# Kernel tuning notes

Hardware: AMD Instinct MI355X
Metric: run time of the kernel (lower is better)

The kernel has to match this reference:

```python
import jax, jax.numpy as jnp
import numpy as np

B, N, D, K = 4, 2048, 128, 32
EPS = 1e-5  # nn.LayerNorm default eps


def _lin(k, fan_in, fan_out):
    kw, kb = jax.random.split(k)
    s = 1.0 / np.sqrt(fan_in)
    w = jax.random.uniform(kw, (fan_in, fan_out), jnp.float32, -s, s)
    b = jax.random.uniform(kb, (fan_out,), jnp.float32, -s, s)
    return w, b


def setup_inputs() -> dict:
    key = jax.random.key(0)
    ks = jax.random.split(key, 3)
    inp = {}
    inp["features"] = jax.random.normal(ks[0], (B, N, D), jnp.float32)
    inp["coords"] = jax.random.uniform(ks[1], (B, N, 3), jnp.float32) * 64.0
    names = [("ql", D, D), ("kl", D, D), ("vl", D, D), ("pl1", 3, D), ("pl2", D, D),
             ("we1", D, D), ("we2", D, D), ("pe1", 3, D), ("pe2", D, D),
             ("sg1", D, D), ("sg2", D, D)]
    k2 = jax.random.split(ks[2], len(names))
    for (nm, fi, fo), kk in zip(names, k2):
        w, b = _lin(kk, fi, fo)
        inp[nm + "_w"] = w
        inp[nm + "_b"] = b
    inp["lnA_g"] = jnp.ones((D,), jnp.float32)
    inp["lnA_b"] = jnp.zeros((D,), jnp.float32)
    inp["lnF_g"] = jnp.ones((D,), jnp.float32)
    inp["lnF_b"] = jnp.zeros((D,), jnp.float32)
    return inp


def _sparsemax_k(z):
    # sparsemax over axis=1 (the K neighbor axis) of [N, K, D]
    zs = -jnp.sort(-z, axis=1)                      # descending sort
    zc = jnp.cumsum(zs, axis=1)
    r = jnp.arange(1, K + 1, dtype=z.dtype)[None, :, None]
    support = (r * zs) > (zc - 1.0)
    kz = jnp.sum(support, axis=1, keepdims=True).astype(jnp.int32)  # >= 1
    tau = (jnp.take_along_axis(zc, kz - 1, axis=1) - 1.0) / kz.astype(z.dtype)
    return jnp.maximum(z - tau, 0.0)


def _sg_prop(x, src, tgt, n):
    # SGConv (K=1) propagation: D^{-1/2}(A+I)D^{-1/2} x with self-loops added
    ar = jnp.arange(n)
    s = jnp.concatenate([src, ar])
    t = jnp.concatenate([tgt, ar])
    deg = jax.ops.segment_sum(jnp.ones(s.shape, x.dtype), t, num_segments=n)
    dinv = jax.lax.rsqrt(deg)
    norm = dinv[s] * dinv[t]
    return jax.ops.segment_sum(x[s] * norm[:, None], t, num_segments=n)


def reference(features, coords,
              ql_w, ql_b, kl_w, kl_b, vl_w, vl_b,
              pl1_w, pl1_b, pl2_w, pl2_b,
              we1_w, we1_b, we2_w, we2_b,
              lnA_g, lnA_b,
              pe1_w, pe1_b, pe2_w, pe2_b,
              sg1_w, sg1_b, sg2_w, sg2_b,
              lnF_g, lnF_b):
    def ln(x, g, b):
        m = jnp.mean(x, axis=-1, keepdims=True)
        v = jnp.var(x, axis=-1, keepdims=True)
        return (x - m) * jax.lax.rsqrt(v + EPS) * g + b

    def one(feat, coord):
        # ---- RNSA: KNN self-attention with positional embedding ----
        d2 = jnp.sum((coord[:, None, :] - coord[None, :, :]) ** 2, axis=-1)  # [N,N]
        _, idx = jax.lax.top_k(-d2, K)                   # [N,K], self included first
        diff = coord[idx] - coord[:, None, :]            # [N,K,3]
        fc = jnp.maximum(diff @ pl1_w + pl1_b, 0.0) @ pl2_w + pl2_b  # [N,K,D]
        pe = fc + feat[idx]
        Q = jnp.maximum(feat @ ql_w + ql_b, 0.0)         # [N,D]
        Kf = jnp.maximum(pe @ kl_w + kl_b, 0.0)          # [N,K,D]
        V = pe @ vl_w + vl_b
        rel = (Kf - Q[:, None, :]) * fc
        w = jnp.maximum(rel @ we1_w + we1_b, 0.0) @ we2_w + we2_b
        w = _sparsemax_k(w)                              # attn_drop is identity (eval)
        x_att = feat + jnp.einsum('nkd,nkd->nd', V, w)   # residual add
        cf = jnp.maximum(coord @ pe1_w + pe1_b, 0.0) @ pe2_w + pe2_b
        x_in = ln(x_att, lnA_g, lnA_b)
        x_pe = x_in + cf
        d2m = d2 + jnp.where(jnp.eye(N, dtype=bool), jnp.inf, 0.0)  # knn_graph: loop=False
        _, idx2 = jax.lax.top_k(-d2m, K)                 # [N,K] neighbors (sources)
        src = idx2.reshape(-1)
        tgt = jnp.repeat(jnp.arange(N), K)
        h = _sg_prop(x_pe, src, tgt, N) @ sg1_w + sg1_b
        h = jnp.maximum(h, 0.0)
        h = _sg_prop(h, src, tgt, N) @ sg2_w + sg2_b     # dropout is identity (eval)
        return ln(h + x_in, lnF_g, lnF_b)

    return jax.vmap(one)(features, coords)
```

## Files before the change

kernel.cpp:

```cpp
#include <hip/hip_runtime.h>
#include <hip/hip_bf16.h>


namespace {
constexpr int BB = 4;
constexpr int NN = 2048;
constexpr int DD = 128;
constexpr int KK = 32;
constexpr float LNEPS = 1e-5f;
constexpr int SH = 136;

constexpr int W_QL = 0, W_KL = 16384, W_VL = 32768, W_PL2 = 49152, W_WE1 = 65536,
              W_WE2 = 81920, W_PE2 = 98304, W_SG1 = 114688, W_SG2 = 131072,
              W_PL1 = 147456, W_PE1 = 147840,
              B_QL = 148224, B_KL = 148352, B_VL = 148480, B_PL1 = 148608, B_PL2 = 148736,
              B_WE1 = 148864, B_WE2 = 148992, B_PE1 = 149120, B_PE2 = 149248,
              B_SG1 = 149376, B_SG2 = 149504,
              LNA_G = 149632, LNA_B = 149760, LNF_G = 149888, LNF_B = 150016;

constexpr long OFF_FEAT  = 0;
constexpr long OFF_Q     = 1l << 20;
constexpr long OFF_XIN   = 3l << 20;
constexpr long OFF_XPE   = 4l << 20;
constexpr long OFF_H1    = 5l << 20;
constexpr long OFF_COORD = 6l << 20;
constexpr long OFF_W     = (6l << 20) + 32768;
constexpr long OFF_IDX   = (6l << 20) + 262144;
}

typedef _Float16 f16;
typedef __attribute__((ext_vector_type(8))) _Float16 half8;
typedef __attribute__((ext_vector_type(4))) float f32x4;

struct WPtrs { const void* p[26]; };

__device__ __forceinline__ f32x4 mfma16h(half8 a, half8 b, f32x4 c) {
  return __builtin_amdgcn_mfma_f32_16x16x32_f16(a, b, c, 0, 0, 0);
}
__device__ __forceinline__ bool bf_inputs(const unsigned* __restrict__ dt) {
  return (dt[0] & 0xFFFFu) != 0u;
}

__global__ __launch_bounds__(256) void k_prep(WPtrs wp,
    const void* __restrict__ feat, const void* __restrict__ coord,
    const unsigned* __restrict__ dt,
    float* __restrict__ featf, float* __restrict__ coordf, float* __restrict__ Wf,
    f16* __restrict__ pkH, f16* __restrict__ pkL) {
  const bool isbf = bf_inputs(dt);
  const int tid = threadIdx.x;
  if (blockIdx.x < 2048) {
    const int nf = BB * NN * DD, nc = BB * NN * 3;
    for (int i = blockIdx.x * 256 + tid; i < nf + nc; i += 2048 * 256) {
      if (i < nf) {
        featf[i] = isbf ? __bfloat162float(((const __hip_bfloat16*)feat)[i])
                        : ((const float*)feat)[i];
      } else {
        const int j = i - nf;
        coordf[j] = isbf ? __bfloat162float(((const __hip_bfloat16*)coord)[j])
                         : ((const float*)coord)[j];
      }
    }
  } else if (blockIdx.x < 2048 + 26) {
    const int sizes[26] = {16384,16384,16384,16384,16384,16384,16384,16384,16384,
                           384,384,
                           128,128,128,128,128,128,128,128,128,128,128,
                           128,128,128,128};
    const int offs[26] = {W_QL,W_KL,W_VL,W_PL2,W_WE1,W_WE2,W_PE2,W_SG1,W_SG2,
                          W_PL1,W_PE1,
                          B_QL,B_KL,B_VL,B_PL1,B_PL2,B_WE1,B_WE2,B_PE1,B_PE2,B_SG1,B_SG2,
                          LNA_G,LNA_B,LNF_G,LNF_B};
    const int t = blockIdx.x - 2048;
    float* dst = Wf + offs[t];
    const int n = sizes[t];
    if (isbf) {
      const __hip_bfloat16* src = (const __hip_bfloat16*)wp.p[t];
      for (int i = tid; i < n; i += 256) dst[i] = __bfloat162float(src[i]);
    } else {
      const float* src = (const float*)wp.p[t];
      for (int i = tid; i < n; i += 256) dst[i] = src[i];
    }
  } else {
    const int wmap[9] = {3, 1, 2, 4, 5, 6, 7, 8, 0};
    const int m = blockIdx.x - 2048 - 26;
    const void* src = wp.p[wmap[m]];
    f16* H = pkH + m * 16384;
    f16* L = pkL + m * 16384;
    for (int f = tid; f < 16384; f += 256) {
      const int j = f & 7, lane = (f >> 3) & 63, ks = (f >> 9) & 3, nt = f >> 11;
      const int k = ks * 32 + ((lane >> 4) << 3) + j, n = nt * 16 + (lane & 15);
      const float v = isbf ? __bfloat162float(((const __hip_bfloat16*)src)[k * 128 + n])
                           : ((const float*)src)[k * 128 + n];
      const f16 h = (f16)v;
      H[f] = h;
      L[f] = (f16)(v - (float)h);
    }
  }
}

__device__ __forceinline__ void mm_core(const f16* sA,
                                        const f16* __restrict__ wH,
                                        const f16* __restrict__ wL,
                                        bool useLoW, int lane, int wv, f32x4 acc[2][2]) {
  const int colq = lane & 15, quad = lane >> 4;
  #pragma unroll
  for (int mt = 0; mt < 2; ++mt) {
    const int arow = mt * 16 + colq;
    f32x4 a0 = {0.f, 0.f, 0.f, 0.f}, a1 = {0.f, 0.f, 0.f, 0.f};
    #pragma unroll
    for (int ks = 0; ks < 4; ++ks) {
      const half8 a = *(const half8*)(sA + arow * SH + ks * 32 + quad * 8);
      const int nt0 = 2 * wv, nt1 = 2 * wv + 1;
      const half8 b0 = *(const half8*)(wH + ((nt0 * 4 + ks) * 64 + lane) * 8);
      const half8 b1 = *(const half8*)(wH + ((nt1 * 4 + ks) * 64 + lane) * 8);
      a0 = mfma16h(a, b0, a0);
      a1 = mfma16h(a, b1, a1);
      if (useLoW) {
        const half8 bl0 = *(const half8*)(wL + ((nt0 * 4 + ks) * 64 + lane) * 8);
        const half8 bl1 = *(const half8*)(wL + ((nt1 * 4 + ks) * 64 + lane) * 8);
        a0 = mfma16h(a, bl0, a0);
        a1 = mfma16h(a, bl1, a1);
      }
    }
    acc[mt][0] = a0;
    acc[mt][1] = a1;
  }
}

__device__ __forceinline__ void h_store2(f16* A, int row0, int col, float v0, float v1) {
  A[row0 * SH + col] = (f16)v0;
  A[(row0 + 1) * SH + col] = (f16)v1;
}

__device__ __forceinline__ void h_store_row16(f16* A, int row, int c0, const float* v) {
  half8 o0, o1;
  #pragma unroll
  for (int e = 0; e < 8; ++e) { o0[e] = (f16)v[e]; o1[e] = (f16)v[8 + e]; }
  *(half8*)(A + row * SH + c0) = o0;
  *(half8*)(A + row * SH + c0 + 8) = o1;
}

__global__ __launch_bounds__(256) void k_knn_q(const float* __restrict__ coordf,
                                               const float* __restrict__ featf,
                                               const float* __restrict__ Wf,
                                               const f16* __restrict__ pkH,
                                               const f16* __restrict__ pkL,
                                               const unsigned* __restrict__ dt,
                                               int* __restrict__ idx1, int* __restrict__ idx2,
                                               float* __restrict__ Qm) {
  __shared__ __align__(16) unsigned char smem[NN * 3 * 4 + 4 * 33 * 4];
  const int tid = threadIdx.x;
  if (blockIdx.x < 2048) {
    float* cs = (float*)smem;
    int (*tops)[33] = (int(*)[33])(smem + NN * 3 * 4);
    const int wv = tid >> 6, lane = tid & 63;
    const int blk = blockIdx.x;
    const int b = blk >> 9;
    const int i = ((blk & 511) << 2) + wv;
    const float* cb = coordf + (long)b * NN * 3;
    for (int t = tid; t < NN * 3 / 4; t += 256) ((float4*)cs)[t] = ((const float4*)cb)[t];
    __syncthreads();
    const float qx = cs[i*3+0], qy = cs[i*3+1], qz = cs[i*3+2];
    float v[32];
    unsigned removed = 0u;
    float m1v = 1e30f, m2v = 1e30f; int m1j = 0x7fffffff, m2j = 0x7fffffff;
    #pragma unroll
    for (int m = 0; m < 32; m++) {
      const int j = m * 64 + lane;
      const float dx = cs[j*3+0] - qx, dy = cs[j*3+1] - qy, dz = cs[j*3+2] - qz;
      const float d2 = __fadd_rn(__fadd_rn(__fmul_rn(dx,dx), __fmul_rn(dy,dy)), __fmul_rn(dz,dz));
      v[m] = d2;
      if (d2 < m1v)      { m2v = m1v; m2j = m1j; m1v = d2; m1j = j; }
      else if (d2 < m2v) { m2v = d2; m2j = j; }
    }
    bool dirty = false;
    for (int s = 0; s < 33; s++) {
      float mv = m1v; int mj = m1j;
      #pragma unroll
      for (int off = 1; off < 64; off <<= 1) {
        const float ov = __shfl_xor(mv, off, 64);
        const int   oj = __shfl_xor(mj, off, 64);
        if (ov < mv || (ov == mv && oj < mj)) { mv = ov; mj = oj; }
      }
      if (lane == 0) tops[wv][s] = mj;
      if ((mj & 63) == lane) {
        removed |= 1u << (mj >> 6);
        if (!dirty) { m1v = m2v; m1j = m2j; dirty = true; }
        else {
          m1v = 1e30f; m1j = 0x7fffffff; m2v = 1e30f; m2j = 0x7fffffff;
          #pragma unroll
          for (int m = 0; m < 32; m++) {
            if (!((removed >> m) & 1u)) {
              const float d2 = v[m]; const int j = m * 64 + lane;
              if (d2 < m1v)      { m2v = m1v; m2j = m1j; m1v = d2; m1j = j; }
              else if (d2 < m2v) { m2v = d2; m2j = j; }
            }
          }
          dirty = false;
        }
      }
    }
    const unsigned long long sm = __ballot(lane < 33 && tops[wv][lane] == i);
    const int p = sm ? (__ffsll((long long)sm) - 1) : 32;
    if (lane < KK) {
      const long g = (long)b * NN + i;
      idx1[g * KK + lane] = tops[wv][lane];
      idx2[g * KK + lane] = tops[wv][lane + (lane >= p ? 1 : 0)];
    }
  } else {
    f16* AH = (f16*)smem;
    const int lane = tid & 63, wv = tid >> 6;
    const int colq = lane & 15, quad = lane >> 4;
    const bool useLoW = !bf_inputs(dt);
    const int row8 = tid >> 3, c0 = (tid & 7) * 16;
    const long gg0 = (long)(blockIdx.x - 2048) * 32;
    float s[16];
    const float* sp = featf + (gg0 + row8) * DD + c0;
    #pragma unroll
    for (int e = 0; e < 16; e += 4) {
      const float4 vv = *(const float4*)(sp + e);
      s[e] = vv.x; s[e+1] = vv.y; s[e+2] = vv.z; s[e+3] = vv.w;
    }
    h_store_row16(AH, row8, c0, s);
    __syncthreads();
    f32x4 acc[2][2];
    mm_core(AH, pkH + 8*16384, pkL + 8*16384, useLoW, lane, wv, acc);
    #pragma unroll
    for (int ntl = 0; ntl < 2; ++ntl) {
      const int col = (2*wv + ntl)*16 + colq;
      const float bv = Wf[B_QL + col];
      #pragma unroll
      for (int mt = 0; mt < 2; ++mt) {
        const int rowb = mt*16 + quad*4;
        #pragma unroll
        for (int r = 0; r < 4; ++r)
          Qm[(gg0 + rowb + r) * DD + col] = fmaxf(acc[mt][ntl][r] + bv, 0.f);
      }
    }
  }
}

__global__ __launch_bounds__(256, 4) void k_attn(const float* __restrict__ featf,
                                              const float* __restrict__ coordf,
                                              const float* __restrict__ Qm,
                                              const int* __restrict__ idx1,
                                              const float* __restrict__ Wf,
                                              const f16* __restrict__ pkH,
                                              const f16* __restrict__ pkL,
                                              const unsigned* __restrict__ dt,
                                              float* __restrict__ x_in) {
  __shared__ __align__(16) f16 AH[KK*SH], CH[KK*SH];
  __shared__ int nb[KK];
  const int tid = threadIdx.x;
  const int lane = tid & 63, wv = tid >> 6;
  const int colq = lane & 15, quad = lane >> 4;
  const int g = blockIdx.x; const int i = g & (NN - 1); const int b = g >> 11;
  const long bN = (long)b * NN;
  const bool useLoW = !bf_inputs(dt);
  if (tid < KK) nb[tid] = idx1[(long)g * KK + tid];
  const int row8 = tid >> 3, c0 = (tid & 7) * 16;

  {
    const int j = idx1[(long)g * KK + row8];
    const float* cb = coordf + (long)b * NN * 3;
    const float dx = cb[j*3+0] - cb[i*3+0], dy = cb[j*3+1] - cb[i*3+1], dz = cb[j*3+2] - cb[i*3+2];
    float t1v[16];
    #pragma unroll
    for (int c4 = 0; c4 < 4; ++c4) {
      const int cc = c0 + c4*4;
      const float4 w0 = *(const float4*)(Wf + W_PL1 + cc);
      const float4 w1 = *(const float4*)(Wf + W_PL1 + 128 + cc);
      const float4 w2 = *(const float4*)(Wf + W_PL1 + 256 + cc);
      const float4 bp = *(const float4*)(Wf + B_PL1 + cc);
      t1v[c4*4+0] = fmaxf(fmaf(dz,w2.x,fmaf(dy,w1.x,fmaf(dx,w0.x,bp.x))), 0.f);
      t1v[c4*4+1] = fmaxf(fmaf(dz,w2.y,fmaf(dy,w1.y,fmaf(dx,w0.y,bp.y))), 0.f);
      t1v[c4*4+2] = fmaxf(fmaf(dz,w2.z,fmaf(dy,w1.z,fmaf(dx,w0.z,bp.z))), 0.f);
      t1v[c4*4+3] = fmaxf(fmaf(dz,w2.w,fmaf(dy,w1.w,fmaf(dx,w0.w,bp.w))), 0.f);
    }
    h_store_row16(AH, row8, c0, t1v);
  }
  __syncthreads();
  f32x4 acc[2][2];
  float fc[2][2][4];
  {
    float pfeat[2][2][4];
    #pragma unroll
    for (int ntl = 0; ntl < 2; ++ntl) {
      const int col = (2*wv + ntl)*16 + colq;
      #pragma unroll
      for (int mt = 0; mt < 2; ++mt) {
        const int rowb = mt*16 + quad*4;
        #pragma unroll
        for (int r = 0; r < 4; ++r)
          pfeat[ntl][mt][r] = featf[(bN + nb[rowb + r]) * DD + col];
      }
    }
    mm_core(AH, pkH + 0*16384, pkL + 0*16384, useLoW, lane, wv, acc);
    #pragma unroll
    for (int ntl = 0; ntl < 2; ++ntl) {
      const int col = (2*wv + ntl)*16 + colq;
      const float bv = Wf[B_PL2 + col];
      #pragma unroll
      for (int mt = 0; mt < 2; ++mt) {
        const int rowb = mt*16 + quad*4;
        float pe[4];
        #pragma unroll
        for (int r = 0; r < 4; ++r) {
          const float f = acc[mt][ntl][r] + bv;
          fc[mt][ntl][r] = f;
          pe[r] = f + pfeat[ntl][mt][r];
        }
        h_store2(CH, rowb + 0, col, pe[0], pe[1]);
        h_store2(CH, rowb + 2, col, pe[2], pe[3]);
      }
    }
  }
  __syncthreads();
  {
    const float qv0 = Qm[(bN + i) * DD + (2*wv + 0)*16 + colq];
    const float qv1 = Qm[(bN + i) * DD + (2*wv + 1)*16 + colq];
    mm_core(CH, pkH + 1*16384, pkL + 1*16384, useLoW, lane, wv, acc);
    #pragma unroll
    for (int ntl = 0; ntl < 2; ++ntl) {
      const int col = (2*wv + ntl)*16 + colq;
      const float bv = Wf[B_KL + col];
      const float qv = ntl ? qv1 : qv0;
      #pragma unroll
      for (int mt = 0; mt < 2; ++mt) {
        const int rowb = mt*16 + quad*4;
        float rel[4];
        #pragma unroll
        for (int r = 0; r < 4; ++r) {
          const float kf = fmaxf(acc[mt][ntl][r] + bv, 0.f);
          rel[r] = (kf - qv) * fc[mt][ntl][r];
        }
        h_store2(AH, rowb + 0, col, rel[0], rel[1]);
        h_store2(AH, rowb + 2, col, rel[2], rel[3]);
      }
    }
  }
  f32x4 Vacc[2][2];
  mm_core(CH, pkH + 2*16384, pkL + 2*16384, useLoW, lane, wv, Vacc);
  __syncthreads();
  {
    mm_core(AH, pkH + 3*16384, pkL + 3*16384, useLoW, lane, wv, acc);
    #pragma unroll
    for (int ntl = 0; ntl < 2; ++ntl) {
      const int col = (2*wv + ntl)*16 + colq;
      const float bv = Wf[B_WE1 + col];
      #pragma unroll
      for (int mt = 0; mt < 2; ++mt) {
        const int rowb = mt*16 + quad*4;
        h_store2(CH, rowb + 0, col,
                 fmaxf(acc[mt][ntl][0] + bv, 0.f), fmaxf(acc[mt][ntl][1] + bv, 0.f));
        h_store2(CH, rowb + 2, col,
                 fmaxf(acc[mt][ntl][2] + bv, 0.f), fmaxf(acc[mt][ntl][3] + bv, 0.f));
      }
    }
  }
  __syncthreads();
  float* XR = (float*)AH;
  const float res0 = featf[(bN + i) * DD + (2*wv + 0)*16 + colq];
  const float res1 = featf[(bN + i) * DD + (2*wv + 1)*16 + colq];
  f32x4 Wacc[2][2];
  mm_core(CH, pkH + 4*16384, pkL + 4*16384, useLoW, lane, wv, Wacc);

  #pragma unroll
  for (int ntl = 0; ntl < 2; ++ntl) {
    const int col = (2*wv + ntl)*16 + colq;
    const float bw = Wf[B_WE2 + col];
    const float bvv = Wf[B_VL + col];
    float z[8], Vv[8];
    #pragma unroll
    for (int mt = 0; mt < 2; ++mt)
      #pragma unroll
      for (int r = 0; r < 4; ++r) {
        z[mt*4+r]  = Wacc[mt][ntl][r] + bw;
        Vv[mt*4+r] = Vacc[mt][ntl][r] + bvv;
      }
    float S = 0.f;
    #pragma unroll
    for (int e = 0; e < 8; ++e) S += z[e];
    S += __shfl_xor(S, 16, 64); S += __shfl_xor(S, 32, 64);
    float tau = (S - 1.0f) * (1.0f / 32.0f);
    int cnt = 32;
    for (int it = 0; it < 40; ++it) {
      float s = 0.f; int c = 0;
      #pragma unroll
      for (int e = 0; e < 8; ++e) { if (z[e] > tau) { s += z[e]; c++; } }
      s += __shfl_xor(s, 16, 64); s += __shfl_xor(s, 32, 64);
      c += __shfl_xor(c, 16, 64); c += __shfl_xor(c, 32, 64);
      const float ntau = (s - 1.0f) / (float)c;
      const int changed = (c != cnt);
      cnt = c; tau = ntau;
      if (!__any(changed)) break;
    }
    float pv = 0.f;
    #pragma unroll
    for (int e = 0; e < 8; ++e) pv = fmaf(fmaxf(z[e] - tau, 0.f), Vv[e], pv);
    pv += __shfl_xor(pv, 16, 64); pv += __shfl_xor(pv, 32, 64);
    if (quad == 0) XR[col] = (ntl ? res1 : res0) + pv;
  }
  __syncthreads();
  {
    const float xa0 = XR[2*lane], xa1 = XR[2*lane + 1];
    float sm = xa0 + xa1;
    float s2 = fmaf(xa0, xa0, xa1 * xa1);
    #pragma unroll
    for (int off = 1; off < 64; off <<= 1) {
      sm += __shfl_xor(sm, off, 64);
      s2 += __shfl_xor(s2, off, 64);
    }
    const float m = sm * (1.f/128.f);
    const float var = s2 * (1.f/128.f) - m * m;
    const float rstd = rsqrtf(var + LNEPS);
    if (tid < DD) {
      const float xin = (XR[tid] - m) * rstd * Wf[LNA_G + tid] + Wf[LNA_B + tid];
      x_in[(bN + i) * DD + tid] = xin;
    }
  }
}

__global__ __launch_bounds__(256) void k_pe(const float* __restrict__ x_in,
                                            const float* __restrict__ coordf,
                                            const float* __restrict__ Wf,
                                            const f16* __restrict__ pkH,
                                            const f16* __restrict__ pkL,
                                            const unsigned* __restrict__ dt,
                                            float* __restrict__ x_pe) {
  __shared__ __align__(16) f16 AH[KK*SH];
  const int tid = threadIdx.x;
  const int lane = tid & 63, wv = tid >> 6;
  const int colq = lane & 15, quad = lane >> 4;
  const bool useLoW = !bf_inputs(dt);
  const int row8 = tid >> 3, c0 = (tid & 7) * 16;
  const long gg0 = (long)blockIdx.x * 32;
  const long gr = gg0 + row8;
  const int b = (int)(gr >> 11), i = (int)(gr & (NN - 1));

  {
    const float* cp = coordf + ((long)b * NN + i) * 3;
    const float cx = cp[0], cy = cp[1], cz = cp[2];
    float tv[16];
    #pragma unroll
    for (int c4 = 0; c4 < 4; ++c4) {
      const int cc = c0 + c4*4;
      const float4 w0 = *(const float4*)(Wf + W_PE1 + cc);
      const float4 w1 = *(const float4*)(Wf + W_PE1 + 128 + cc);
      const float4 w2 = *(const float4*)(Wf + W_PE1 + 256 + cc);
      const float4 bp = *(const float4*)(Wf + B_PE1 + cc);
      tv[c4*4+0] = fmaxf(fmaf(cz,w2.x,fmaf(cy,w1.x,fmaf(cx,w0.x,bp.x))), 0.f);
      tv[c4*4+1] = fmaxf(fmaf(cz,w2.y,fmaf(cy,w1.y,fmaf(cx,w0.y,bp.y))), 0.f);
      tv[c4*4+2] = fmaxf(fmaf(cz,w2.z,fmaf(cy,w1.z,fmaf(cx,w0.z,bp.z))), 0.f);
      tv[c4*4+3] = fmaxf(fmaf(cz,w2.w,fmaf(cy,w1.w,fmaf(cx,w0.w,bp.w))), 0.f);
    }
    h_store_row16(AH, row8, c0, tv);
  }
  __syncthreads();
  f32x4 acc[2][2];
  mm_core(AH, pkH + 5*16384, pkL + 5*16384, useLoW, lane, wv, acc);
  #pragma unroll
  for (int ntl = 0; ntl < 2; ++ntl) {
    const int col = (2*wv + ntl)*16 + colq;
    const float bv = Wf[B_PE2 + col];
    #pragma unroll
    for (int mt = 0; mt < 2; ++mt) {
      const int rowb = mt*16 + quad*4;
      #pragma unroll
      for (int r = 0; r < 4; ++r)
        x_pe[(gg0 + rowb + r) * DD + col] =
            x_in[(gg0 + rowb + r) * DD + col] + acc[mt][ntl][r] + bv;
    }
  }
}

__global__ __launch_bounds__(256) void k_sg1(const float* __restrict__ x_pe,
                                             const int* __restrict__ idx2,
                                             const float* __restrict__ Wf,
                                             const f16* __restrict__ pkH,
                                             const f16* __restrict__ pkL,
                                             const unsigned* __restrict__ dt,
                                             float* __restrict__ h1) {
  __shared__ __align__(16) f16 AH[KK*SH];
  __shared__ int nb2[32][KK];
  const int tid = threadIdx.x;
  const int lane = tid & 63, wv = tid >> 6;
  const int colq = lane & 15, quad = lane >> 4;
  const bool useLoW = !bf_inputs(dt);
  const int row8 = tid >> 3, c0 = (tid & 7) * 16;
  const long gg0 = (long)blockIdx.x * 32;
  const long bN = (gg0 >> 11) << 11;
  for (int t = tid; t < 32 * KK; t += 256)
    nb2[t >> 5][t & 31] = idx2[(gg0 + (t >> 5)) * KK + (t & 31)];
  __syncthreads();
  float s[16];
  {
    const float* sp = x_pe + (gg0 + row8) * DD + c0;
    #pragma unroll
    for (int e = 0; e < 16; e += 4) {
      const float4 v = *(const float4*)(sp + e);
      s[e] = v.x; s[e+1] = v.y; s[e+2] = v.z; s[e+3] = v.w;
    }
  }
  for (int k = 0; k < KK; ++k) {
    const float* np_ = x_pe + (bN + nb2[row8][k]) * DD + c0;
    #pragma unroll
    for (int e = 0; e < 16; e += 4) {
      const float4 v = *(const float4*)(np_ + e);
      s[e] += v.x; s[e+1] += v.y; s[e+2] += v.z; s[e+3] += v.w;
    }
  }
  #pragma unroll
  for (int e = 0; e < 16; ++e) s[e] *= (1.f / 33.f);
  h_store_row16(AH, row8, c0, s);
  __syncthreads();
  f32x4 acc[2][2];
  mm_core(AH, pkH + 6*16384, pkL + 6*16384, useLoW, lane, wv, acc);
  #pragma unroll
  for (int ntl = 0; ntl < 2; ++ntl) {
    const int col = (2*wv + ntl)*16 + colq;
    const float bv = Wf[B_SG1 + col];
    #pragma unroll
    for (int mt = 0; mt < 2; ++mt) {
      const int rowb = mt*16 + quad*4;
      #pragma unroll
      for (int r = 0; r < 4; ++r)
        h1[(gg0 + rowb + r) * DD + col] = fmaxf(acc[mt][ntl][r] + bv, 0.f);
    }
  }
}

__global__ __launch_bounds__(256) void k_sg2(const float* __restrict__ h1,
                                             const int* __restrict__ idx2,
                                             const float* __restrict__ x_in,
                                             const float* __restrict__ Wf,
                                             const f16* __restrict__ pkH,
                                             const f16* __restrict__ pkL,
                                             const unsigned* __restrict__ dt,
                                             void* __restrict__ out) {
  __shared__ __align__(16) f16 AH[KK*SH];
  __shared__ float Yf[KK][132];
  __shared__ int nb2[32][KK];
  const int tid = threadIdx.x;
  const int lane = tid & 63, wv = tid >> 6;
  const int colq = lane & 15, quad = lane >> 4;
  const bool isbf = bf_inputs(dt);
  const bool useLoW = !isbf;
  const int row8 = tid >> 3, c0 = (tid & 7) * 16;
  const long gg0 = (long)blockIdx.x * 32;
  const long bN = (gg0 >> 11) << 11;
  for (int t = tid; t < 32 * KK; t += 256)
    nb2[t >> 5][t & 31] = idx2[(gg0 + (t >> 5)) * KK + (t & 31)];
  __syncthreads();
  float s[16];
  {
    const float* sp = h1 + (gg0 + row8) * DD + c0;
    #pragma unroll
    for (int e = 0; e < 16; e += 4) {
      const float4 v = *(const float4*)(sp + e);
      s[e] = v.x; s[e+1] = v.y; s[e+2] = v.z; s[e+3] = v.w;
    }
  }
  for (int k = 0; k < KK; ++k) {
    const float* np_ = h1 + (bN + nb2[row8][k]) * DD + c0;
    #pragma unroll
    for (int e = 0; e < 16; e += 4) {
      const float4 v = *(const float4*)(np_ + e);
      s[e] += v.x; s[e+1] += v.y; s[e+2] += v.z; s[e+3] += v.w;
    }
  }
  #pragma unroll
  for (int e = 0; e < 16; ++e) s[e] *= (1.f / 33.f);
  h_store_row16(AH, row8, c0, s);
  __syncthreads();
  f32x4 acc[2][2];
  mm_core(AH, pkH + 7*16384, pkL + 7*16384, useLoW, lane, wv, acc);
  #pragma unroll
  for (int ntl = 0; ntl < 2; ++ntl) {
    const int col = (2*wv + ntl)*16 + colq;
    const float bv = Wf[B_SG2 + col];
    #pragma unroll
    for (int mt = 0; mt < 2; ++mt) {
      const int rowb = mt*16 + quad*4;
      #pragma unroll
      for (int r = 0; r < 4; ++r)
        Yf[rowb + r][col] = acc[mt][ntl][r] + bv + x_in[(gg0 + rowb + r) * DD + col];
    }
  }
  __syncthreads();
  float y[16];
  #pragma unroll
  for (int e = 0; e < 16; ++e) y[e] = Yf[row8][c0 + e];
  float sm = 0.f, s2 = 0.f;
  #pragma unroll
  for (int e = 0; e < 16; ++e) { sm += y[e]; s2 = fmaf(y[e], y[e], s2); }
  #pragma unroll
  for (int off = 1; off < 8; off <<= 1) {
    sm += __shfl_xor(sm, off, 64);
    s2 += __shfl_xor(s2, off, 64);
  }
  const float m = sm * (1.f/128.f);
  const float var = s2 * (1.f/128.f) - m * m;
  const float rstd = rsqrtf(var + LNEPS);
  const long gr = gg0 + row8;
  #pragma unroll
  for (int e = 0; e < 16; ++e) {
    const float o = (y[e] - m) * rstd * Wf[LNF_G + c0 + e] + Wf[LNF_B + c0 + e];
    if (isbf) ((__hip_bfloat16*)out)[gr * DD + c0 + e] = __float2bfloat16(o);
    else      ((float*)out)[gr * DD + c0 + e] = o;
  }
}

extern "C" void kernel_launch(void* const* d_in, const int* in_sizes, int n_in,
                              void* d_out, int out_size, void* d_ws, size_t ws_size,
                              hipStream_t stream) {
  float* ws = (float*)d_ws;
  float* featf  = ws + OFF_FEAT;
  float* Qm     = ws + OFF_Q;
  float* x_in   = ws + OFF_XIN;
  float* x_pe   = ws + OFF_XPE;
  float* h1     = ws + OFF_H1;
  float* coordf = ws + OFF_COORD;
  float* Wf     = ws + OFF_W;
  int* idx1 = (int*)(ws + OFF_IDX);
  int* idx2 = idx1 + (long)BB * NN * KK;
  f16* pkH = (f16*)(idx2 + (long)BB * NN * KK);
  f16* pkL = pkH + 9 * 16384;
  const unsigned* dt = (const unsigned*)d_in[24];

  WPtrs wp;
  const int map[26] = {2,4,6,10,12,14,18,20,22, 8,16,
                       3,5,7,9,11,13,15,17,19,21,23,
                       24,25,26,27};
  for (int t = 0; t < 26; t++) wp.p[t] = d_in[map[t]];

  k_prep<<<2048 + 26 + 9, 256, 0, stream>>>(wp, d_in[0], d_in[1], dt,
                                            featf, coordf, Wf, pkH, pkL);
  k_knn_q<<<BB * NN / 4 + BB * NN / 32, 256, 0, stream>>>(coordf, featf, Wf, pkH, pkL, dt,
                                                          idx1, idx2, Qm);
  k_attn<<<BB * NN, 256, 0, stream>>>(featf, coordf, Qm, idx1, Wf, pkH, pkL, dt, x_in);
  k_pe<<<BB * NN / 32, 256, 0, stream>>>(x_in, coordf, Wf, pkH, pkL, dt, x_pe);
  k_sg1<<<BB * NN / 32, 256, 0, stream>>>(x_pe, idx2, Wf, pkH, pkL, dt, h1);
  k_sg2<<<BB * NN / 32, 256, 0, stream>>>(h1, idx2, x_in, Wf, pkH, pkL, dt, (void*)d_out);
}
```

Baseline: 460.2 us.

## Move KNN search into prep kernel, split Q projection into its own kernel

```diff
diff --git a/kernel.cpp b/kernel.cpp
--- a/kernel.cpp
+++ b/kernel.cpp
@@ -45,7 +45,9 @@
     const void* __restrict__ feat, const void* __restrict__ coord,
     const unsigned* __restrict__ dt,
     float* __restrict__ featf, float* __restrict__ coordf, float* __restrict__ Wf,
-    f16* __restrict__ pkH, f16* __restrict__ pkL) {
+    f16* __restrict__ pkH, f16* __restrict__ pkL,
+    int* __restrict__ idx1, int* __restrict__ idx2) {
+  __shared__ __align__(16) unsigned char smem[NN * 3 * 4 + 4 * 33 * 4];
   const bool isbf = bf_inputs(dt);
   const int tid = threadIdx.x;
   if (blockIdx.x < 2048) {
@@ -79,7 +81,7 @@
       const float* src = (const float*)wp.p[t];
       for (int i = tid; i < n; i += 256) dst[i] = src[i];
     }
-  } else {
+  } else if (blockIdx.x < 2048 + 26 + 9) {
     const int wmap[9] = {3, 1, 2, 4, 5, 6, 7, 8, 0};
     const int m = blockIdx.x - 2048 - 26;
     const void* src = wp.p[wmap[m]];
@@ -94,70 +96,27 @@
       H[f] = h;
       L[f] = (f16)(v - (float)h);
     }
-  }
-}
-
-__device__ __forceinline__ void mm_core(const f16* sA,
-                                        const f16* __restrict__ wH,
-                                        const f16* __restrict__ wL,
-                                        bool useLoW, int lane, int wv, f32x4 acc[2][2]) {
-  const int colq = lane & 15, quad = lane >> 4;
-  #pragma unroll
-  for (int mt = 0; mt < 2; ++mt) {
-    const int arow = mt * 16 + colq;
-    f32x4 a0 = {0.f, 0.f, 0.f, 0.f}, a1 = {0.f, 0.f, 0.f, 0.f};
-    #pragma unroll
-    for (int ks = 0; ks < 4; ++ks) {
-      const half8 a = *(const half8*)(sA + arow * SH + ks * 32 + quad * 8);
-      const int nt0 = 2 * wv, nt1 = 2 * wv + 1;
-      const half8 b0 = *(const half8*)(wH + ((nt0 * 4 + ks) * 64 + lane) * 8);
-      const half8 b1 = *(const half8*)(wH + ((nt1 * 4 + ks) * 64 + lane) * 8);
-      a0 = mfma16h(a, b0, a0);
-      a1 = mfma16h(a, b1, a1);
-      if (useLoW) {
-        const half8 bl0 = *(const half8*)(wL + ((nt0 * 4 + ks) * 64 + lane) * 8);
-        const half8 bl1 = *(const half8*)(wL + ((nt1 * 4 + ks) * 64 + lane) * 8);
-        a0 = mfma16h(a, bl0, a0);
-        a1 = mfma16h(a, bl1, a1);
-      }
-    }
-    acc[mt][0] = a0;
-    acc[mt][1] = a1;
-  }
-}
-
-__device__ __forceinline__ void h_store2(f16* A, int row0, int col, float v0, float v1) {
-  A[row0 * SH + col] = (f16)v0;
-  A[(row0 + 1) * SH + col] = (f16)v1;
-}
-
-__device__ __forceinline__ void h_store_row16(f16* A, int row, int c0, const float* v) {
-  half8 o0, o1;
-  #pragma unroll
-  for (int e = 0; e < 8; ++e) { o0[e] = (f16)v[e]; o1[e] = (f16)v[8 + e]; }
-  *(half8*)(A + row * SH + c0) = o0;
-  *(half8*)(A + row * SH + c0 + 8) = o1;
-}
-
-__global__ __launch_bounds__(256) void k_knn_q(const float* __restrict__ coordf,
-                                               const float* __restrict__ featf,
-                                               const float* __restrict__ Wf,
-                                               const f16* __restrict__ pkH,
-                                               const f16* __restrict__ pkL,
-                                               const unsigned* __restrict__ dt,
-                                               int* __restrict__ idx1, int* __restrict__ idx2,
-                                               float* __restrict__ Qm) {
-  __shared__ __align__(16) unsigned char smem[NN * 3 * 4 + 4 * 33 * 4];
-  const int tid = threadIdx.x;
-  if (blockIdx.x < 2048) {
+  } else {
     float* cs = (float*)smem;
     int (*tops)[33] = (int(*)[33])(smem + NN * 3 * 4);
     const int wv = tid >> 6, lane = tid & 63;
-    const int blk = blockIdx.x;
+    const int blk = blockIdx.x - 2048 - 26 - 9;
     const int b = blk >> 9;
     const int i = ((blk & 511) << 2) + wv;
-    const float* cb = coordf + (long)b * NN * 3;
-    for (int t = tid; t < NN * 3 / 4; t += 256) ((float4*)cs)[t] = ((const float4*)cb)[t];
+    const long cbase = (long)b * NN * 3;
+    for (int t = tid; t < NN * 3 / 4; t += 256) {
+      float4 v;
+      if (isbf) {
+        const ushort4 u = ((const ushort4*)((const __hip_bfloat16*)coord + cbase))[t];
+        v.x = __uint_as_float((unsigned)u.x << 16);
+        v.y = __uint_as_float((unsigned)u.y << 16);
+        v.z = __uint_as_float((unsigned)u.z << 16);
+        v.w = __uint_as_float((unsigned)u.w << 16);
+      } else {
+        v = ((const float4*)((const float*)coord + cbase))[t];
+      }
+      ((float4*)cs)[t] = v;
+    }
     __syncthreads();
     const float qx = cs[i*3+0], qy = cs[i*3+1], qz = cs[i*3+2];
     float v[32];
@@ -206,35 +165,85 @@
       idx1[g * KK + lane] = tops[wv][lane];
       idx2[g * KK + lane] = tops[wv][lane + (lane >= p ? 1 : 0)];
     }
-  } else {
-    f16* AH = (f16*)smem;
-    const int lane = tid & 63, wv = tid >> 6;
-    const int colq = lane & 15, quad = lane >> 4;
-    const bool useLoW = !bf_inputs(dt);
-    const int row8 = tid >> 3, c0 = (tid & 7) * 16;
-    const long gg0 = (long)(blockIdx.x - 2048) * 32;
-    float s[16];
-    const float* sp = featf + (gg0 + row8) * DD + c0;
-    #pragma unroll
-    for (int e = 0; e < 16; e += 4) {
-      const float4 vv = *(const float4*)(sp + e);
-      s[e] = vv.x; s[e+1] = vv.y; s[e+2] = vv.z; s[e+3] = vv.w;
-    }
-    h_store_row16(AH, row8, c0, s);
-    __syncthreads();
-    f32x4 acc[2][2];
-    mm_core(AH, pkH + 8*16384, pkL + 8*16384, useLoW, lane, wv, acc);
-    #pragma unroll
-    for (int ntl = 0; ntl < 2; ++ntl) {
-      const int col = (2*wv + ntl)*16 + colq;
-      const float bv = Wf[B_QL + col];
-      #pragma unroll
-      for (int mt = 0; mt < 2; ++mt) {
-        const int rowb = mt*16 + quad*4;
-        #pragma unroll
-        for (int r = 0; r < 4; ++r)
-          Qm[(gg0 + rowb + r) * DD + col] = fmaxf(acc[mt][ntl][r] + bv, 0.f);
-      }
+  }
+}
+
+__device__ __forceinline__ void mm_core(const f16* sA,
+                                        const f16* __restrict__ wH,
+                                        const f16* __restrict__ wL,
+                                        bool useLoW, int lane, int wv, f32x4 acc[2][2]) {
+  const int colq = lane & 15, quad = lane >> 4;
+  #pragma unroll
+  for (int mt = 0; mt < 2; ++mt) {
+    const int arow = mt * 16 + colq;
+    f32x4 a0 = {0.f, 0.f, 0.f, 0.f}, a1 = {0.f, 0.f, 0.f, 0.f};
+    #pragma unroll
+    for (int ks = 0; ks < 4; ++ks) {
+      const half8 a = *(const half8*)(sA + arow * SH + ks * 32 + quad * 8);
+      const int nt0 = 2 * wv, nt1 = 2 * wv + 1;
+      const half8 b0 = *(const half8*)(wH + ((nt0 * 4 + ks) * 64 + lane) * 8);
+      const half8 b1 = *(const half8*)(wH + ((nt1 * 4 + ks) * 64 + lane) * 8);
+      a0 = mfma16h(a, b0, a0);
+      a1 = mfma16h(a, b1, a1);
+      if (useLoW) {
+        const half8 bl0 = *(const half8*)(wL + ((nt0 * 4 + ks) * 64 + lane) * 8);
+        const half8 bl1 = *(const half8*)(wL + ((nt1 * 4 + ks) * 64 + lane) * 8);
+        a0 = mfma16h(a, bl0, a0);
+        a1 = mfma16h(a, bl1, a1);
+      }
+    }
+    acc[mt][0] = a0;
+    acc[mt][1] = a1;
+  }
+}
+
+__device__ __forceinline__ void h_store2(f16* A, int row0, int col, float v0, float v1) {
+  A[row0 * SH + col] = (f16)v0;
+  A[(row0 + 1) * SH + col] = (f16)v1;
+}
+
+__device__ __forceinline__ void h_store_row16(f16* A, int row, int c0, const float* v) {
+  half8 o0, o1;
+  #pragma unroll
+  for (int e = 0; e < 8; ++e) { o0[e] = (f16)v[e]; o1[e] = (f16)v[8 + e]; }
+  *(half8*)(A + row * SH + c0) = o0;
+  *(half8*)(A + row * SH + c0 + 8) = o1;
+}
+
+__global__ __launch_bounds__(256) void k_q(const float* __restrict__ featf,
+                                           const float* __restrict__ Wf,
+                                           const f16* __restrict__ pkH,
+                                           const f16* __restrict__ pkL,
+                                           const unsigned* __restrict__ dt,
+                                           float* __restrict__ Qm) {
+  __shared__ __align__(16) f16 AH[KK*SH];
+  const int tid = threadIdx.x;
+  const int lane = tid & 63, wv = tid >> 6;
+  const int colq = lane & 15, quad = lane >> 4;
+  const bool useLoW = !bf_inputs(dt);
+  const int row8 = tid >> 3, c0 = (tid & 7) * 16;
+  const long gg0 = (long)blockIdx.x * 32;
+  float s[16];
+  const float* sp = featf + (gg0 + row8) * DD + c0;
+  #pragma unroll
+  for (int e = 0; e < 16; e += 4) {
+    const float4 vv = *(const float4*)(sp + e);
+    s[e] = vv.x; s[e+1] = vv.y; s[e+2] = vv.z; s[e+3] = vv.w;
+  }
+  h_store_row16(AH, row8, c0, s);
+  __syncthreads();
+  f32x4 acc[2][2];
+  mm_core(AH, pkH + 8*16384, pkL + 8*16384, useLoW, lane, wv, acc);
+  #pragma unroll
+  for (int ntl = 0; ntl < 2; ++ntl) {
+    const int col = (2*wv + ntl)*16 + colq;
+    const float bv = Wf[B_QL + col];
+    #pragma unroll
+    for (int mt = 0; mt < 2; ++mt) {
+      const int rowb = mt*16 + quad*4;
+      #pragma unroll
+      for (int r = 0; r < 4; ++r)
+        Qm[(gg0 + rowb + r) * DD + col] = fmaxf(acc[mt][ntl][r] + bv, 0.f);
     }
   }
 }
@@ -633,10 +642,9 @@
                        24,25,26,27};
   for (int t = 0; t < 26; t++) wp.p[t] = d_in[map[t]];
 
-  k_prep<<<2048 + 26 + 9, 256, 0, stream>>>(wp, d_in[0], d_in[1], dt,
-                                            featf, coordf, Wf, pkH, pkL);
-  k_knn_q<<<BB * NN / 4 + BB * NN / 32, 256, 0, stream>>>(coordf, featf, Wf, pkH, pkL, dt,
-                                                          idx1, idx2, Qm);
+  k_prep<<<2048 + 26 + 9 + 2048, 256, 0, stream>>>(wp, d_in[0], d_in[1], dt,
+                                                   featf, coordf, Wf, pkH, pkL, idx1, idx2);
+  k_q<<<BB * NN / 32, 256, 0, stream>>>(featf, Wf, pkH, pkL, dt, Qm);
   k_attn<<<BB * NN, 256, 0, stream>>>(featf, coordf, Qm, idx1, Wf, pkH, pkL, dt, x_in);
   k_pe<<<BB * NN / 32, 256, 0, stream>>>(x_in, coordf, Wf, pkH, pkL, dt, x_pe);
   k_sg1<<<BB * NN / 32, 256, 0, stream>>>(x_pe, idx2, Wf, pkH, pkL, dt, h1);
```

Measured after the change: 447.3 us. 2.8% less time.
